# Kernel tuning notes

Hardware: AMD Instinct MI355X
Metric: run time of the kernel (lower is better)

The kernel has to match this reference:

```python
import jax, jax.numpy as jnp
import numpy as np

KSIZE = 5
KNUM = 16
STRIDE = 1


def setup_inputs() -> dict:
    key = jax.random.key(0)
    k1, k2 = jax.random.split(key, 2)
    mu_in = jax.random.normal(k1, (16, 28, 28, 1), dtype=jnp.float32)
    # w_mu init: normal(0, 0.05); w_sigma init: constant -2.2 (as in build())
    w_mu = 0.05 * jax.random.normal(k2, (KSIZE, KSIZE, 1, KNUM), dtype=jnp.float32)
    w_sigma = jnp.full((KNUM,), -2.2, dtype=jnp.float32)
    return {"mu_in": mu_in, "w_mu": w_mu, "w_sigma": w_sigma}


def reference(mu_in, w_mu, w_sigma):
    # mu path: standard NHWC conv, VALID padding
    mu_out = jax.lax.conv_general_dilated(
        mu_in, w_mu, window_strides=(STRIDE, STRIDE), padding='VALID',
        dimension_numbers=('NHWC', 'HWIO', 'NHWC'))

    # Sigma path: extract patches -> [B, P, F] matrix (patch ordering is a
    # permutation of TF's, which leaves the Gram matrix X X^T invariant)
    patches = jax.lax.conv_general_dilated_patches(
        mu_in, filter_shape=(KSIZE, KSIZE), window_strides=(STRIDE, STRIDE),
        padding='VALID', dimension_numbers=('NHWC', 'HWIO', 'NHWC'))
    B = mu_in.shape[0]
    X = patches.reshape(B, -1, patches.shape[-1])          # [B, P, F]
    G = jnp.einsum('bpf,bqf->bpq', X, X)                   # [B, P, P]

    # per-output-channel softplus scale, broadcast to [B, P, P, KNUM]
    scale = jnp.log1p(jnp.exp(w_sigma))                    # log(1 + exp(w_sigma))
    Sigma = scale * G[..., None]                           # [B, P, P, KNUM]

    Sigma = jnp.where(jnp.isnan(Sigma), jnp.zeros_like(Sigma), Sigma)
    Sigma = jnp.where(jnp.isinf(Sigma), jnp.zeros_like(Sigma), Sigma)

    # tf.linalg.set_diag acts on the LAST TWO dims -> [P, KNUM] matrices:
    # abs the entries Sigma[:, :, i, i] for i < min(P, KNUM)
    m = min(Sigma.shape[-2], Sigma.shape[-1])
    i = jnp.arange(m)
    Sigma = Sigma.at[..., i, i].set(jnp.abs(Sigma[..., i, i]))
    return (mu_out, Sigma)
```

## Files before the change

kernel.cpp:

```cpp
#include <hip/hip_runtime.h>
#include <math.h>

#define BATCH 16
#define H     28
#define W     28
#define KS    5
#define KN    16
#define OHW   24
#define P     576
#define PP    (P * P)
#define NTHR  256
#define MU_OUT_ELEMS (BATCH * P * KN)
#define G_ELEMS      (BATCH * PP)
#define SIG_F4       (BATCH * PP * KN / 4)

typedef float vfloat4 __attribute__((ext_vector_type(4)));

__global__ __launch_bounds__(NTHR) void gram_kernel(
    const float* __restrict__ mu_in,
    const float* __restrict__ w_mu,
    float* __restrict__ G,
    float* __restrict__ out)
{
    __shared__ float mu_s[H * W];
    __shared__ float wmu_s[KS * KS * KN];

    const int tid  = threadIdx.x;
    const int wave = tid >> 6;
    const int lane = tid & 63;

    const int blocks_per_b = P / 4;
    const int b = blockIdx.x / blocks_per_b;
    const int p = (blockIdx.x % blocks_per_b) * 4 + wave;

    const float* mu_b = mu_in + b * (H * W);
    for (int i = tid; i < H * W; i += NTHR) mu_s[i] = mu_b[i];
    for (int i = tid; i < KS * KS * KN; i += NTHR) wmu_s[i] = w_mu[i];
    __syncthreads();

    const int ph = p / OHW;
    const int pw = p % OHW;

    float Xp[KS * KS];
    #pragma unroll
    for (int kh = 0; kh < KS; ++kh)
        #pragma unroll
        for (int kw = 0; kw < KS; ++kw)
            Xp[kh * KS + kw] = mu_s[(ph + kh) * W + (pw + kw)];

    if (lane < KN) {
        float acc = 0.f;
        #pragma unroll
        for (int j = 0; j < KS * KS; ++j)
            acc += Xp[j] * wmu_s[j * KN + lane];
        out[(b * P + p) * KN + lane] = acc;
    }

    float* grow = G + (size_t)(b * P + p) * P;
    #pragma unroll
    for (int r = 0; r < 9; ++r) {
        const int q  = r * 64 + lane;
        const int qh = q / OHW;
        const int qw = q % OHW;
        const float* mq = &mu_s[qh * W + qw];
        float acc = 0.f;
        #pragma unroll
        for (int kh = 0; kh < KS; ++kh)
            #pragma unroll
            for (int kw = 0; kw < KS; ++kw)
                acc += Xp[kh * KS + kw] * mq[kh * W + kw];
        grow[q] = acc;
    }
}

__global__ __launch_bounds__(NTHR) void bcast_kernel(
    const float* __restrict__ G,
    const float* __restrict__ w_sigma,
    float* __restrict__ out)
{
    const int tid0 = (int)(blockIdx.x * NTHR + threadIdx.x);
    const int S    = (int)(gridDim.x * NTHR);
    const unsigned c = (unsigned)(tid0 & 3);

    const float sc0 = log1pf(expf(w_sigma[4 * c + 0]));
    const float sc1 = log1pf(expf(w_sigma[4 * c + 1]));
    const float sc2 = log1pf(expf(w_sigma[4 * c + 2]));
    const float sc3 = log1pf(expf(w_sigma[4 * c + 3]));

    vfloat4* sig = (vfloat4*)(out + MU_OUT_ELEMS);

    for (int F = tid0; F < SIG_F4; F += S) {
        const unsigned idx = (unsigned)F >> 2;
        const float g = G[idx];
        vfloat4 v = { g * sc0, g * sc1, g * sc2, g * sc3 };
        const unsigned q = idx % (unsigned)P;
        if ((q >> 2) == c) {
            const unsigned j = q & 3;
            v[j] = fabsf(v[j]);
        }
        sig[F] = v;
    }
}

__global__ __launch_bounds__(NTHR) void vdp_fused_kernel(
    const float* __restrict__ mu_in,
    const float* __restrict__ w_mu,
    const float* __restrict__ w_sigma,
    float* __restrict__ out)
{
    __shared__ float mu_s[H * W];
    __shared__ float wmu_s[KS * KS * KN];
    __shared__ float sp_s[KN];

    const int tid  = threadIdx.x;
    const int wave = tid >> 6;
    const int lane = tid & 63;

    const int blocks_per_b = P / 4;
    const int b = blockIdx.x / blocks_per_b;
    const int p = (blockIdx.x % blocks_per_b) * 4 + wave;

    const float* mu_b = mu_in + b * (H * W);
    for (int i = tid; i < H * W; i += NTHR) mu_s[i] = mu_b[i];
    for (int i = tid; i < KS * KS * KN; i += NTHR) wmu_s[i] = w_mu[i];
    if (tid < KN) sp_s[tid] = log1pf(expf(w_sigma[tid]));
    __syncthreads();

    const int ph = p / OHW;
    const int pw = p % OHW;

    float Xp[KS * KS];
    #pragma unroll
    for (int kh = 0; kh < KS; ++kh)
        #pragma unroll
        for (int kw = 0; kw < KS; ++kw)
            Xp[kh * KS + kw] = mu_s[(ph + kh) * W + (pw + kw)];

    if (lane < KN) {
        float acc = 0.f;
        #pragma unroll
        for (int j = 0; j < KS * KS; ++j)
            acc += Xp[j] * wmu_s[j * KN + lane];
        out[(b * P + p) * KN + lane] = acc;
    }

    const int c = lane & 3;
    const float sc0 = sp_s[4 * c + 0];
    const float sc1 = sp_s[4 * c + 1];
    const float sc2 = sp_s[4 * c + 2];
    const float sc3 = sp_s[4 * c + 3];

    vfloat4* rowp = (vfloat4*)(out + MU_OUT_ELEMS + (size_t)(b * P + p) * (P * KN));

    float g[9];
    #pragma unroll
    for (int r = 0; r < 9; ++r) {
        const int q  = r * 64 + lane;
        const int qh = q / OHW;
        const int qw = q % OHW;
        const float* mq = &mu_s[qh * W + qw];
        float acc = 0.f;
        #pragma unroll
        for (int kh = 0; kh < KS; ++kh)
            #pragma unroll
            for (int kw = 0; kw < KS; ++kw)
                acc += Xp[kh * KS + kw] * mq[kh * W + kw];
        g[r] = acc;
    }

    float gq[36];
    #pragma unroll
    for (int s = 0; s < 36; ++s)
        gq[s] = __shfl(g[s >> 2], 16 * (s & 3) + (lane >> 2));

    #pragma unroll
    for (int s = 0; s < 36; ++s) {
        vfloat4 v = { gq[s] * sc0, gq[s] * sc1, gq[s] * sc2, gq[s] * sc3 };
        if (s == 0) {
            const int qq = lane >> 2;
            if ((qq >> 2) == c) {
                const int r2 = qq & 3;
                v[r2] = fabsf(v[r2]);
            }
        }
        rowp[s * 64 + lane] = v;
    }
}

extern "C" void kernel_launch(void* const* d_in, const int* in_sizes, int n_in,
                              void* d_out, int out_size, void* d_ws, size_t ws_size,
                              hipStream_t stream) {
    const float* mu_in   = (const float*)d_in[0];
    const float* w_mu    = (const float*)d_in[1];
    const float* w_sigma = (const float*)d_in[2];
    float* out = (float*)d_out;

    const size_t g_bytes = (size_t)G_ELEMS * sizeof(float);
    if (d_ws != nullptr && ws_size >= g_bytes) {
        float* G = (float*)d_ws;
        gram_kernel<<<dim3(BATCH * P / 4), dim3(NTHR), 0, stream>>>(
            mu_in, w_mu, G, out);
        bcast_kernel<<<dim3(768), dim3(NTHR), 0, stream>>>(
            G, w_sigma, out);
    } else {
        vdp_fused_kernel<<<dim3(BATCH * P / 4), dim3(NTHR), 0, stream>>>(
            mu_in, w_mu, w_sigma, out);
    }
}
```

Baseline: 384.5 us.

## Restructure broadcast kernel into row-based double-buffered G loads and vector stores

The broadcast kernel now has each 512-block grid handle whole Gram rows. Each lane loads 9 G values per row, with two rows in flight as a software pipeline so loads overlap the vec4 stores. This replaces the grid-stride loop, which loaded each G element four times and paid a modulo per element. The diagonal abs test is hoisted to a per-lane flag. The risk is less memory-level parallelism, since the grid is smaller and each thread holds only two rows of loads in flight.

```diff
diff --git a/kernel.cpp b/kernel.cpp
--- a/kernel.cpp
+++ b/kernel.cpp
@@ -10,9 +10,10 @@
 #define P     576
 #define PP    (P * P)
 #define NTHR  256
+#define NROWS (BATCH * P)
 #define MU_OUT_ELEMS (BATCH * P * KN)
 #define G_ELEMS      (BATCH * PP)
-#define SIG_F4       (BATCH * PP * KN / 4)
+#define BGRID 512
 
 typedef float vfloat4 __attribute__((ext_vector_type(4)));
 
@@ -78,28 +79,56 @@
     const float* __restrict__ w_sigma,
     float* __restrict__ out)
 {
-    const int tid0 = (int)(blockIdx.x * NTHR + threadIdx.x);
-    const int S    = (int)(gridDim.x * NTHR);
-    const unsigned c = (unsigned)(tid0 & 3);
+    const int tid  = threadIdx.x;
+    const int wave = tid >> 6;
+    const int lane = tid & 63;
+    const int qg   = lane >> 2;
+    const int c    = lane & 3;
 
     const float sc0 = log1pf(expf(w_sigma[4 * c + 0]));
     const float sc1 = log1pf(expf(w_sigma[4 * c + 1]));
     const float sc2 = log1pf(expf(w_sigma[4 * c + 2]));
     const float sc3 = log1pf(expf(w_sigma[4 * c + 3]));
 
-    vfloat4* sig = (vfloat4*)(out + MU_OUT_ELEMS);
-
-    for (int F = tid0; F < SIG_F4; F += S) {
-        const unsigned idx = (unsigned)F >> 2;
-        const float g = G[idx];
-        vfloat4 v = { g * sc0, g * sc1, g * sc2, g * sc3 };
-        const unsigned q = idx % (unsigned)P;
-        if ((q >> 2) == c) {
-            const unsigned j = q & 3;
-            v[j] = fabsf(v[j]);
-        }
-        sig[F] = v;
-    }
+    vfloat4* sig4 = (vfloat4*)(out + MU_OUT_ELEMS);
+    const bool dlane = ((qg >> 2) == c);
+    const int  dcomp = qg & 3;
+
+#define LOADG(garr, rr)                                                      \
+    {                                                                        \
+        const float* gp_ = G + (size_t)(rr) * P + wave * 144 + qg;           \
+        _Pragma("unroll")                                                    \
+        for (int j = 0; j < 9; ++j) garr[j] = gp_[j * 16];                   \
+    }
+
+#define BURST(garr, rr)                                                      \
+    {                                                                        \
+        vfloat4* dst_ = sig4 + (size_t)(rr) * (P * KN / 4) + wave * 576 + lane; \
+        _Pragma("unroll")                                                    \
+        for (int j = 0; j < 9; ++j) {                                        \
+            const float g_ = garr[j];                                        \
+            vfloat4 v_ = { g_ * sc0, g_ * sc1, g_ * sc2, g_ * sc3 };         \
+            if (wave == 0 && j == 0) {                                       \
+                if (dlane) v_[dcomp] = fabsf(v_[dcomp]);                     \
+            }                                                                \
+            dst_[j * 64] = v_;                                               \
+        }                                                                    \
+    }
+
+    float ga[9], gb[9];
+    const int bx = (int)blockIdx.x;
+
+    LOADG(ga, bx);
+    #pragma unroll 1
+    for (int i = 0; i < 9; ++i) {
+        const int ra = bx + 1024 * i;
+        LOADG(gb, ra + 512);
+        BURST(ga, ra);
+        if (i != 8) LOADG(ga, ra + 1024);
+        BURST(gb, ra + 512);
+    }
+#undef LOADG
+#undef BURST
 }
 
 __global__ __launch_bounds__(NTHR) void vdp_fused_kernel(
@@ -200,7 +229,7 @@
         float* G = (float*)d_ws;
         gram_kernel<<<dim3(BATCH * P / 4), dim3(NTHR), 0, stream>>>(
             mu_in, w_mu, G, out);
-        bcast_kernel<<<dim3(768), dim3(NTHR), 0, stream>>>(
+        bcast_kernel<<<dim3(BGRID), dim3(NTHR), 0, stream>>>(
             G, w_sigma, out);
     } else {
         vdp_fused_kernel<<<dim3(BATCH * P / 4), dim3(NTHR), 0, stream>>>(
```

Measured after the change: 372.5 us. -3.1%, faster.
